# Kernel tuning notes

Measured on AMD Instinct MI355X. Metric: run time of the kernel, lower is better.

The kernel has to match this reference:

```python
import jax, jax.numpy as jnp
import numpy as np

N = 40000
IN_DIM = 2000
HID = 512
OUT_DIM = 30
E = 400000


def setup_inputs() -> dict:
    key = jax.random.key(0)
    k1, k2, k3, k4, k5, k6 = jax.random.split(key, 6)
    features = jax.random.normal(k1, (N, IN_DIM), dtype=jnp.float32)
    edge_index = jax.random.randint(k2, (2, E), 0, N, dtype=jnp.int64)
    # xavier_normal_(gain=1.414): std = gain * sqrt(2/(fan_in+fan_out))
    W1 = jax.random.normal(k3, (IN_DIM, HID), dtype=jnp.float32) * (1.414 * np.sqrt(2.0 / (IN_DIM + HID)))
    W2 = jax.random.normal(k4, (HID, OUT_DIM), dtype=jnp.float32) * (1.414 * np.sqrt(2.0 / (HID + OUT_DIM)))
    att_src = jax.random.normal(k5, (HID,), dtype=jnp.float32) * (1.414 * np.sqrt(2.0 / (1 + HID)))
    att_dst = jax.random.normal(k6, (HID,), dtype=jnp.float32) * (1.414 * np.sqrt(2.0 / (1 + HID)))
    return {"features": features, "W1": W1, "W2": W2,
            "att_src": att_src, "att_dst": att_dst, "edge_index": edge_index}


def _gat_propagate(x_proj, alpha_src, alpha_dst, src, dst, n_nodes):
    """GATConv message+aggregate (heads=1, aggr='add').
    x_proj: [N, C] projected features; alpha_src/alpha_dst: [N] per-node scores.
    """
    score = jax.nn.sigmoid(alpha_src[src] + alpha_dst[dst])          # [E]
    # segment softmax over destination neighborhoods (PyG softmax)
    seg_max = jax.ops.segment_max(score, dst, num_segments=n_nodes)  # [N]
    e = jnp.exp(score - seg_max[dst])                                # [E]
    seg_sum = jax.ops.segment_sum(e, dst, num_segments=n_nodes)     # [N]
    alpha = e / (seg_sum[dst] + 1e-16)                               # [E]
    msg = x_proj[src] * alpha[:, None]                               # [E, C] gather + scale
    return jax.ops.segment_sum(msg, dst, num_segments=n_nodes)      # [N, C] scatter-add


def _stagate_forward(features, W1, W2, att_src, att_dst, src, dst):
    n = features.shape[0]
    # conv1: attention=True (computes its own alpha)
    x1 = features @ W1                                # [N, HID]
    a_src = x1 @ att_src                              # [N]
    a_dst = x1 @ att_dst                              # [N]
    h1 = jax.nn.elu(_gat_propagate(x1, a_src, a_dst, src, dst, n))
    # conv2: attention=False -> just linear projection (heads=1 mean)
    h2 = h1 @ W2                                      # [N, OUT_DIM]
    # conv3: weights tied to W2^T, attention tied to conv1's alphas
    x3 = h2 @ W2.T                                    # [N, HID]
    h3 = jax.nn.elu(_gat_propagate(x3, a_src, a_dst, src, dst, n))
    # conv4: attention=False, weights tied to W1^T
    h4 = h3 @ W1.T                                    # [N, IN_DIM]
    return h2, h4


def reference(features, W1, W2, att_src, att_dst, edge_index):
    src = edge_index[0]
    dst = edge_index[1]
    return _stagate_forward(features, W1, W2, att_src, att_dst, src, dst)
```

## Files before the change

### kernel.cpp

```cpp
#include <hip/hip_runtime.h>
#include <cstdint>

#define NNODES 40000
#define INDIM 2000
#define HIDD 512
#define ODIM 30
#define NEDGES 400000
#define KPAD 2048

typedef short bf16x8 __attribute__((ext_vector_type(8)));
typedef float f32x4 __attribute__((ext_vector_type(4)));

__device__ __forceinline__ float bf2f(ushort u){ union{unsigned int i; float f;} x; x.i = ((unsigned int)u)<<16; return x.f; }
__device__ __forceinline__ ushort f2bf(float v){ union{float f; unsigned int u;} x; x.f=v; unsigned int r = x.u + 0x7fffu + ((x.u>>16)&1u); return (ushort)(r>>16); }

__device__ __forceinline__ int xcd_swz(int orig, int nwg){
  int q = nwg >> 3, r = nwg & 7;
  int xcd = orig & 7;
  int idx = orig >> 3;
  return (xcd < r ? xcd*(q+1) : r*(q+1) + (xcd-r)*q) + idx;
}

__global__ __launch_bounds__(256) void cast_feat_kernel(const float* __restrict__ src, ushort* __restrict__ dstb){
  int c = blockIdx.x*256 + threadIdx.x;
  int row = c >> 8, kc = c & 255;
  bf16x8 o;
  if (kc < INDIM/8) {
    const float* p = src + (size_t)row*INDIM + kc*8;
    #pragma unroll
    for (int j=0;j<8;++j) o[j] = (short)f2bf(p[j]);
  } else {
    #pragma unroll
    for (int j=0;j<8;++j) o[j] = 0;
  }
  *(bf16x8*)(dstb + (size_t)row*KPAD + kc*8) = o;
}

__global__ __launch_bounds__(256) void cast_w1_kernel(const float* __restrict__ W1, ushort* __restrict__ W1b, ushort* __restrict__ W1t){
  int idx = blockIdx.x*256 + threadIdx.x;
  if (idx >= INDIM*HIDD) return;
  int r = idx >> 9, c = idx & 511;
  ushort b = f2bf(W1[idx]);
  W1b[idx] = b;
  W1t[(size_t)c*KPAD + r] = b;
}

__global__ __launch_bounds__(256) void cast_w2_kernel(const float* __restrict__ W2, ushort* __restrict__ W2p, ushort* __restrict__ W2tc){
  int idx = blockIdx.x*256 + threadIdx.x;
  if (idx >= HIDD*32) return;
  int k = idx >> 5, c = idx & 31;
  float val = (c < ODIM) ? W2[k*ODIM + c] : 0.f;
  ushort b = f2bf(val);
  W2p[k*32 + c] = b;
  W2tc[c*HIDD + k] = b;
}

__global__ __launch_bounds__(256) void hist_kernel(const int* __restrict__ dst, int* __restrict__ deg){
  int e = blockIdx.x*256 + threadIdx.x;
  if (e < NEDGES) atomicAdd(&deg[dst[e]], 1);
}

__global__ __launch_bounds__(1024) void scan_kernel(const int* __restrict__ deg, int* __restrict__ row_ptr){
  __shared__ int part[1024];
  const int t = threadIdx.x;
  const int base = t * 40;
  int v[40];
  int s = 0;
  if (base < NNODES) {
    const int4* dp = (const int4*)(deg + base);
    #pragma unroll
    for (int j=0;j<10;++j){
      int4 d = dp[j];
      v[4*j+0] = s; s += d.x;
      v[4*j+1] = s; s += d.y;
      v[4*j+2] = s; s += d.z;
      v[4*j+3] = s; s += d.w;
    }
  } else {
    #pragma unroll
    for (int j=0;j<40;++j) v[j] = 0;
  }
  part[t] = s;
  __syncthreads();
  #pragma unroll
  for (int off=1; off<1024; off<<=1){
    int x = (t >= off) ? part[t-off] : 0;
    __syncthreads();
    part[t] += x;
    __syncthreads();
  }
  int offset = (t > 0) ? part[t-1] : 0;
  #pragma unroll
  for (int j=0;j<40;++j){
    int i = base + j;
    if (i <= NNODES) row_ptr[i] = offset + v[j];
  }
}

__global__ __launch_bounds__(256) void place_kernel(const int* __restrict__ src, const int* __restrict__ dst,
    const int* __restrict__ row_ptr, int* __restrict__ cursor, int* __restrict__ csr_src){
  int e = blockIdx.x*256 + threadIdx.x;
  if (e >= NEDGES) return;
  int d = dst[e];
  int pos = row_ptr[d] + atomicAdd(&cursor[d], 1);
  csr_src[pos] = src[e];
}

#define P_MID  asm volatile("" ::: "memory"); __builtin_amdgcn_s_barrier(); \
               asm volatile("s_waitcnt lgkmcnt(0)" ::: "memory"); \
               __builtin_amdgcn_sched_barrier(0); __builtin_amdgcn_s_setprio(1);
#define P_END  __builtin_amdgcn_s_setprio(0); asm volatile("" ::: "memory"); \
               __builtin_amdgcn_s_barrier(); __builtin_amdgcn_sched_barrier(0);
#define P_ENDW __builtin_amdgcn_s_setprio(0); \
               asm volatile("s_waitcnt vmcnt(4)" ::: "memory"); \
               asm volatile("" ::: "memory"); __builtin_amdgcn_s_barrier(); \
               __builtin_amdgcn_sched_barrier(0);

template<typename OutT>
__global__ __launch_bounds__(512, 2) void gemm8_kernel(
    const ushort* __restrict__ A, const ushort* __restrict__ Bt,
    OutT* __restrict__ C, int M, int N, int K, int ldc, int nwg, int cshift)
{
  __shared__ __align__(16) char smem[131072];
  ushort* Al = (ushort*)smem;
  ushort* Bl = (ushort*)(smem + 65536);
  const int tid = threadIdx.x;
  const int lane = tid & 63;
  const int w = tid >> 6;
  const int wm = w >> 2, wn = w & 3;
  const int s = xcd_swz(blockIdx.x, nwg);
  const int row0 = (s >> cshift) << 8;
  const int col0 = (s & ((1 << cshift) - 1)) << 8;
  const int NT = K >> 6;

  f32x4 acc[8][4] = {};
  bf16x8 a[4][2], b[4][2];

  auto stage = [&](bool isA, int kt, int h){
    const ushort* G = isA ? A : Bt;
    int base = isA ? row0 : col0;
    int lim  = isA ? M : N;
    ushort* L = (isA ? Al : Bl) + ((kt & 1) << 14);
    if (kt >= NT) kt -= NT;
    #pragma unroll
    for (int it = 0; it < 2; ++it){
      int ch = tid + (it << 9);
      int rl = (h << 7) + (ch >> 3);
      int cs = ch & 7;
      int gr = base + rl; gr = gr < lim ? gr : lim - 1;
      int gc = (kt << 6) + ((cs ^ (rl & 7)) << 3);
      __builtin_amdgcn_global_load_lds(
        (const __attribute__((address_space(1))) unsigned int*)(G + (size_t)gr*K + gc),
        (__attribute__((address_space(3))) unsigned int*)(L + rl*64 + cs*8), 16, 0, 0);
    }
  };
  auto lda = [&](int buf, int mf, int kk) -> bf16x8 {
    int rl = wm*128 + mf*16 + (lane & 15);
    int ko = kk*32 + ((lane >> 4) << 3);
    return *(const bf16x8*)&Al[(buf << 14) + rl*64 + (ko ^ ((rl & 7) << 3))];
  };
  auto ldb = [&](int buf, int nf, int kk) -> bf16x8 {
    int rl = wn*64 + nf*16 + (lane & 15);
    int ko = kk*32 + ((lane >> 4) << 3);
    return *(const bf16x8*)&Bl[(buf << 14) + rl*64 + (ko ^ ((rl & 7) << 3))];
  };
  auto mfma_q = [&](int mbase, int nbase){
    #pragma unroll
    for (int i=0;i<4;++i)
      #pragma unroll
      for (int j=0;j<2;++j)
        #pragma unroll
        for (int kk=0;kk<2;++kk)
          acc[mbase+i][nbase+j] = __builtin_amdgcn_mfma_f32_16x16x32_bf16(
              a[i][kk], b[nbase+j][kk], acc[mbase+i][nbase+j], 0, 0, 0);
  };

  stage(false, 0, 0); stage(false, 0, 1);
  stage(true , 0, 0); stage(true , 0, 1);
  stage(false, 1, 0); stage(false, 1, 1);
  asm volatile("s_waitcnt vmcnt(4)" ::: "memory");
  asm volatile("" ::: "memory");
  __builtin_amdgcn_s_barrier();
  __builtin_amdgcn_sched_barrier(0);

  const int NT2 = NT >> 1;
  for (int t = 0; t < NT2; ++t){
    const int kt0 = 2*t, kt1 = 2*t + 1;
    #pragma unroll
    for (int i=0;i<4;++i){ a[i][0]=lda(0,i,0); a[i][1]=lda(0,i,1); }
    #pragma unroll
    for (int j=0;j<2;++j){ b[j][0]=ldb(0,j,0); b[j][1]=ldb(0,j,1); }
    stage(true, kt1, 0);
    P_MID; mfma_q(0,0); P_END;
    #pragma unroll
    for (int j=2;j<4;++j){ b[j][0]=ldb(0,j,0); b[j][1]=ldb(0,j,1); }
    stage(true, kt1, 1);
    P_MID; mfma_q(0,2); P_END;
    #pragma unroll
    for (int i=0;i<4;++i){ a[i][0]=lda(0,4+i,0); a[i][1]=lda(0,4+i,1); }
    stage(false, kt0+2, 0);
    P_MID; mfma_q(4,0); P_END;
    stage(false, kt0+2, 1);
    P_MID; mfma_q(4,2); P_ENDW;
    #pragma unroll
    for (int i=0;i<4;++i){ a[i][0]=lda(1,i,0); a[i][1]=lda(1,i,1); }
    #pragma unroll
    for (int j=0;j<2;++j){ b[j][0]=ldb(1,j,0); b[j][1]=ldb(1,j,1); }
    stage(true, kt0+2, 0);
    P_MID; mfma_q(0,0); P_END;
    #pragma unroll
    for (int j=2;j<4;++j){ b[j][0]=ldb(1,j,0); b[j][1]=ldb(1,j,1); }
    stage(true, kt0+2, 1);
    P_MID; mfma_q(0,2); P_END;
    #pragma unroll
    for (int i=0;i<4;++i){ a[i][0]=lda(1,4+i,0); a[i][1]=lda(1,4+i,1); }
    stage(false, kt1+2, 0);
    P_MID; mfma_q(4,0); P_END;
    stage(false, kt1+2, 1);
    P_MID; mfma_q(4,2); P_ENDW;
  }

  asm volatile("s_waitcnt vmcnt(0)" ::: "memory");
  __syncthreads();

  if constexpr (sizeof(OutT)==2) {
    ushort* cs = (ushort*)smem;
    #pragma unroll
    for (int p=0;p<2;++p){
      if (wm == p){
        #pragma unroll
        for (int mf=0;mf<8;++mf)
          #pragma unroll
          for (int nf=0;nf<4;++nf)
            #pragma unroll
            for (int reg=0;reg<4;++reg)
              cs[(mf*16 + ((lane>>4)<<2) + reg)*264 + wn*64 + nf*16 + (lane&15)] = f2bf(acc[mf][nf][reg]);
      }
      __syncthreads();
      #pragma unroll
      for (int it=0; it<8; ++it){
        int ch = tid + it*512;
        int r = ch >> 5, c8 = (ch & 31) * 8;
        int gr = row0 + p*128 + r;
        if (gr < M && col0 + c8 + 8 <= N)
          *(bf16x8*)&((ushort*)C)[(size_t)gr*ldc + col0 + c8] = *(const bf16x8*)&cs[r*264 + c8];
      }
      __syncthreads();
    }
  } else {
    float* cf = (float*)smem;
    #pragma unroll
    for (int p=0;p<4;++p){
      if (wm == (p>>1)){
        int mh = (p & 1) * 4;
        #pragma unroll
        for (int i=0;i<4;++i)
          #pragma unroll
          for (int nf=0;nf<4;++nf)
            #pragma unroll
            for (int reg=0;reg<4;++reg)
              cf[(i*16 + ((lane>>4)<<2) + reg)*260 + wn*64 + nf*16 + (lane&15)] = acc[mh+i][nf][reg];
      }
      __syncthreads();
      #pragma unroll
      for (int it=0; it<8; ++it){
        int ch = tid + it*512;
        int r = ch >> 6, c4 = (ch & 63) * 4;
        int gr = row0 + p*64 + r, gc = col0 + c4;
        if (gr < M && gc + 4 <= N)
          *(f32x4*)&((float*)C)[(size_t)gr*ldc + gc] = *(const f32x4*)&cf[r*260 + c4];
      }
      __syncthreads();
    }
  }
}

__global__ __launch_bounds__(256) void a_kernel(const ushort* __restrict__ x1,
    const float* __restrict__ att_src, const float* __restrict__ att_dst,
    float* __restrict__ a_src, float* __restrict__ a_dst){
  int gid = blockIdx.x*256 + threadIdx.x;
  int row = gid >> 6, lane = gid & 63;
  if (row >= NNODES) return;
  bf16x8 v = *(const bf16x8*)(x1 + (size_t)row*HIDD + lane*8);
  float ps = 0.f, pd = 0.f;
  #pragma unroll
  for (int j=0;j<8;++j){
    float xv = bf2f((ushort)v[j]);
    ps += xv * att_src[lane*8+j];
    pd += xv * att_dst[lane*8+j];
  }
  #pragma unroll
  for (int off=32; off>0; off>>=1){ ps += __shfl_down(ps, off); pd += __shfl_down(pd, off); }
  if (lane == 0){ a_src[row] = ps; a_dst[row] = pd; }
}

__global__ __launch_bounds__(256) void agg_fused_kernel(const ushort* __restrict__ X,
    const int* __restrict__ row_ptr, const int* __restrict__ csr_src,
    const float* __restrict__ a_src, const float* __restrict__ a_dst,
    float* __restrict__ csr_alpha, ushort* __restrict__ outb){
  __shared__ float red[3][64*8];
  __shared__ float albuf[1024];
  int v = blockIdx.x;
  int lane = threadIdx.x & 63;
  int q = threadIdx.x >> 6;
  int p0 = row_ptr[v], p1 = row_ptr[v+1];
  int deg = p1 - p0;

  if (q == 0){
    float ad = a_dst[v];
    float m = -1e30f;
    for (int i = lane; i < deg; i += 64){
      float sc = 1.f/(1.f + __expf(-(a_src[csr_src[p0+i]] + ad)));
      if (i < 1024) albuf[i] = sc;
      m = fmaxf(m, sc);
    }
    #pragma unroll
    for (int off=32; off>0; off>>=1) m = fmaxf(m, __shfl_xor(m, off));
    float sum = 0.f;
    for (int i = lane; i < deg; i += 64){
      float sc = (i < 1024) ? albuf[i]
               : 1.f/(1.f + __expf(-(a_src[csr_src[p0+i]] + ad)));
      float e = __expf(sc - m);
      if (i < 1024) albuf[i] = e;
      sum += e;
    }
    #pragma unroll
    for (int off=32; off>0; off>>=1) sum += __shfl_xor(sum, off);
    float inv = 1.f/(sum + 1e-16f);
    for (int i = lane; i < deg; i += 64){
      float e = (i < 1024) ? albuf[i]
              : __expf(1.f/(1.f + __expf(-(a_src[csr_src[p0+i]] + ad))) - m);
      float al = e * inv;
      if (i < 1024) albuf[i] = al;
      csr_alpha[p0+i] = al;
    }
  }
  __syncthreads();

  float acc[8] = {0.f,0.f,0.f,0.f,0.f,0.f,0.f,0.f};
  for (int p = p0 + q; p < p1; p += 4){
    int i = p - p0;
    int sidx = csr_src[p];
    float al = (i < 1024) ? albuf[i] : csr_alpha[p];
    bf16x8 xv = *(const bf16x8*)(X + (size_t)sidx*HIDD + lane*8);
    #pragma unroll
    for (int j=0;j<8;++j) acc[j] += al * bf2f((ushort)xv[j]);
  }
  if (q > 0){
    #pragma unroll
    for (int j=0;j<8;++j) red[q-1][lane*8+j] = acc[j];
  }
  __syncthreads();
  if (q == 0){
    bf16x8 o;
    #pragma unroll
    for (int j=0;j<8;++j){
      float a = acc[j] + red[0][lane*8+j] + red[1][lane*8+j] + red[2][lane*8+j];
      a = a > 0.f ? a : __expf(a)-1.f;
      o[j] = (short)f2bf(a);
    }
    *(bf16x8*)(outb + (size_t)v*HIDD + lane*8) = o;
  }
}

__global__ __launch_bounds__(256) void mid_kernel(const ushort* __restrict__ h1,
    const ushort* __restrict__ W2tc, float* __restrict__ h2){
  __shared__ ushort h1s[32*512];
  __shared__ ushort w2s[32*512];
  const int t = threadIdx.x;
  const int row0 = blockIdx.x * 32;
  const ushort* g = h1 + (size_t)row0*HIDD;
  #pragma unroll
  for (int it=0; it<8; ++it){
    int ch = t + it*256;
    *(bf16x8*)&h1s[ch*8] = *(const bf16x8*)&g[ch*8];
    *(bf16x8*)&w2s[ch*8] = *(const bf16x8*)&W2tc[ch*8];
  }
  __syncthreads();
  int c = t & 31, rg = t >> 5;
  if (c < ODIM){
    float acc[4] = {0.f,0.f,0.f,0.f};
    for (int k0=0;k0<64;++k0){
      bf16x8 wv = *(const bf16x8*)&w2s[c*512 + k0*8];
      #pragma unroll
      for (int rr=0; rr<4; ++rr){
        bf16x8 hv = *(const bf16x8*)&h1s[(rg*4+rr)*HIDD + k0*8];
        #pragma unroll
        for (int j=0;j<8;++j) acc[rr] += bf2f((ushort)hv[j]) * bf2f((ushort)wv[j]);
      }
    }
    #pragma unroll
    for (int rr=0;rr<4;++rr) h2[(size_t)(row0 + rg*4 + rr)*ODIM + c] = acc[rr];
  }
}

__global__ __launch_bounds__(256) void agg30_kernel(const float* __restrict__ h2,
    const int* __restrict__ row_ptr, const int* __restrict__ csr_src,
    const float* __restrict__ csr_alpha, float* __restrict__ g){
  int gid = blockIdx.x*256 + threadIdx.x;
  int v = gid >> 5, lane = gid & 31;
  if (v >= NNODES) return;
  int p0 = row_ptr[v], p1 = row_ptr[v+1];
  float acc = 0.f;
  if (lane < ODIM){
    for (int p = p0; p < p1; ++p){
      acc += csr_alpha[p] * h2[(size_t)csr_src[p]*ODIM + lane];
    }
  }
  g[(size_t)v*32 + lane] = acc;
}

__global__ __launch_bounds__(256) void g2h3_kernel(const float* __restrict__ g,
    const ushort* __restrict__ W2p, ushort* __restrict__ h3){
  int gid = blockIdx.x*256 + threadIdx.x;
  int row = gid >> 6, lane = gid & 63;
  if (row >= NNODES) return;
  float h[ODIM];
  #pragma unroll
  for (int ci=0; ci<ODIM; ++ci) h[ci] = g[(size_t)row*32 + ci];
  #pragma unroll
  for (int it=0; it<8; ++it){
    int n = it*64 + lane;
    const ushort* wr = W2p + n*32;
    bf16x8 wvv[4];
    #pragma unroll
    for (int q=0;q<4;++q) wvv[q] = *(const bf16x8*)(wr + q*8);
    float acc = 0.f;
    #pragma unroll
    for (int ci=0; ci<ODIM; ++ci) acc += h[ci]*bf2f((ushort)wvv[ci>>3][ci&7]);
    acc = acc > 0.f ? acc : __expf(acc)-1.f;
    h3[(size_t)row*HIDD + n] = f2bf(acc);
  }
}

extern "C" void kernel_launch(void* const* d_in, const int* in_sizes, int n_in,
                              void* d_out, int out_size, void* d_ws, size_t ws_size,
                              hipStream_t stream){
  const float* features = (const float*)d_in[0];
  const float* W1 = (const float*)d_in[1];
  const float* W2 = (const float*)d_in[2];
  const float* att_src = (const float*)d_in[3];
  const float* att_dst = (const float*)d_in[4];
  const int* edge = (const int*)d_in[5];
  const int* esrc = edge;
  const int* edst = edge + NEDGES;

  float* h2 = (float*)d_out;
  float* h4 = h2 + (size_t)NNODES*ODIM;
  char* obase = (char*)h4;
  ushort* featb = (ushort*)obase;
  ushort* x1b   = (ushort*)(obase + 163840000);
  ushort* h1b   = (ushort*)(obase + 204800000);

  char* wbase = (char*)d_ws;
  size_t o = 0;
  auto walloc = [&](size_t bytes)->void*{ void* p = wbase + o; o += (bytes + 255) & ~(size_t)255; return p; };
  ushort* h3b      = (ushort*)walloc((size_t)NNODES*HIDD*2);
  ushort* W1b      = (ushort*)walloc((size_t)INDIM*HIDD*2);
  ushort* W1t      = (ushort*)walloc((size_t)HIDD*KPAD*2);
  ushort* W2p      = (ushort*)walloc(512*32*2);
  ushort* W2tc     = (ushort*)walloc(32*512*2);
  float*  a_src    = (float*)walloc(NNODES*4);
  float*  a_dst    = (float*)walloc(NNODES*4);
  int*    deg      = (int*)walloc(NNODES*4);
  int*    cursor   = (int*)walloc(NNODES*4);
  int*    row_ptr  = (int*)walloc((NNODES+1)*4);
  int*    csr_src  = (int*)walloc(NEDGES*4);
  float*  csr_alpha= (float*)walloc(NEDGES*4);
  float*  gbuf     = (float*)walloc((size_t)NNODES*32*4);

  hipMemsetAsync(deg, 0, NNODES*4, stream);
  hipMemsetAsync(cursor, 0, NNODES*4, stream);
  hipMemsetAsync(W1t, 0, (size_t)HIDD*KPAD*2, stream);

  cast_feat_kernel<<<40000, 256, 0, stream>>>(features, featb);
  cast_w1_kernel<<<(INDIM*HIDD+255)/256, 256, 0, stream>>>(W1, W1b, W1t);
  cast_w2_kernel<<<(HIDD*32+255)/256, 256, 0, stream>>>(W2, W2p, W2tc);
  hist_kernel<<<(NEDGES+255)/256, 256, 0, stream>>>(edst, deg);
  scan_kernel<<<1, 1024, 0, stream>>>(deg, row_ptr);
  place_kernel<<<(NEDGES+255)/256, 256, 0, stream>>>(esrc, edst, row_ptr, cursor, csr_src);

  gemm8_kernel<ushort><<<314, 512, 0, stream>>>(featb, W1t, x1b, NNODES, HIDD, KPAD, HIDD, 314, 1);
  a_kernel<<<10000, 256, 0, stream>>>(x1b, att_src, att_dst, a_src, a_dst);
  agg_fused_kernel<<<NNODES, 256, 0, stream>>>(x1b, row_ptr, csr_src, a_src, a_dst, csr_alpha, h1b);
  mid_kernel<<<NNODES/32, 256, 0, stream>>>(h1b, W2tc, h2);
  agg30_kernel<<<NNODES*32/256, 256, 0, stream>>>(h2, row_ptr, csr_src, csr_alpha, gbuf);
  g2h3_kernel<<<10000, 256, 0, stream>>>(gbuf, W2p, h3b);
  gemm8_kernel<float><<<1256, 512, 0, stream>>>(h3b, W1b, h4, NNODES, INDIM, HIDD, INDIM, 1256, 3);
}
```

Measured before the change: 682.6 us.

## Merge setup kernels, fold scan into GEMM, wave-per-node aggregation, fuse conv3

```diff
diff --git a/kernel.cpp b/kernel.cpp
--- a/kernel.cpp
+++ b/kernel.cpp
@@ -21,89 +21,57 @@
   return (xcd < r ? xcd*(q+1) : r*(q+1) + (xcd-r)*q) + idx;
 }
 
-__global__ __launch_bounds__(256) void cast_feat_kernel(const float* __restrict__ src, ushort* __restrict__ dstb){
-  int c = blockIdx.x*256 + threadIdx.x;
-  int row = c >> 8, kc = c & 255;
-  bf16x8 o;
-  if (kc < INDIM/8) {
-    const float* p = src + (size_t)row*INDIM + kc*8;
-    #pragma unroll
-    for (int j=0;j<8;++j) o[j] = (short)f2bf(p[j]);
+#define SB_FEAT   40000
+#define SB_W1     (SB_FEAT + 4000)
+#define SB_W2     (SB_W1 + 64)
+#define SB_HIST   (SB_W2 + 1563)
+#define SB_PAD    (SB_HIST + 96)
+#define SB_CUR    (SB_PAD + 157)
+
+__global__ __launch_bounds__(256) void setup_kernel(
+    const float* __restrict__ features, const float* __restrict__ W1, const float* __restrict__ W2,
+    const int* __restrict__ edst,
+    ushort* __restrict__ featb, ushort* __restrict__ W1b, ushort* __restrict__ W1t,
+    ushort* __restrict__ W2p, ushort* __restrict__ W2tc,
+    int* __restrict__ deg, int* __restrict__ cursor){
+  int b = blockIdx.x, t = threadIdx.x;
+  if (b < SB_FEAT){
+    int c = b*256 + t;
+    int row = c >> 8, kc = c & 255;
+    bf16x8 o;
+    if (kc < INDIM/8) {
+      const float* p = features + (size_t)row*INDIM + kc*8;
+      #pragma unroll
+      for (int j=0;j<8;++j) o[j] = (short)f2bf(p[j]);
+    } else {
+      #pragma unroll
+      for (int j=0;j<8;++j) o[j] = 0;
+    }
+    *(bf16x8*)(featb + (size_t)row*KPAD + kc*8) = o;
+  } else if (b < SB_W1){
+    int idx = (b - SB_FEAT)*256 + t;
+    int r = idx >> 9, c = idx & 511;
+    ushort bb = f2bf(W1[idx]);
+    W1b[idx] = bb;
+    W1t[(size_t)c*KPAD + r] = bb;
+  } else if (b < SB_W2){
+    int idx = (b - SB_W1)*256 + t;
+    int k = idx >> 5, c = idx & 31;
+    float val = (c < ODIM) ? W2[k*ODIM + c] : 0.f;
+    ushort bb = f2bf(val);
+    W2p[k*32 + c] = bb;
+    W2tc[c*HIDD + k] = bb;
+  } else if (b < SB_HIST){
+    int e = (b - SB_W2)*256 + t;
+    if (e < NEDGES) atomicAdd(&deg[edst[e]], 1);
+  } else if (b < SB_PAD){
+    int z = (b - SB_HIST)*256 + t;
+    int c = z / 48, r = 2000 + (z - c*48);
+    W1t[(size_t)c*KPAD + r] = 0;
   } else {
-    #pragma unroll
-    for (int j=0;j<8;++j) o[j] = 0;
-  }
-  *(bf16x8*)(dstb + (size_t)row*KPAD + kc*8) = o;
-}
-
-__global__ __launch_bounds__(256) void cast_w1_kernel(const float* __restrict__ W1, ushort* __restrict__ W1b, ushort* __restrict__ W1t){
-  int idx = blockIdx.x*256 + threadIdx.x;
-  if (idx >= INDIM*HIDD) return;
-  int r = idx >> 9, c = idx & 511;
-  ushort b = f2bf(W1[idx]);
-  W1b[idx] = b;
-  W1t[(size_t)c*KPAD + r] = b;
-}
-
-__global__ __launch_bounds__(256) void cast_w2_kernel(const float* __restrict__ W2, ushort* __restrict__ W2p, ushort* __restrict__ W2tc){
-  int idx = blockIdx.x*256 + threadIdx.x;
-  if (idx >= HIDD*32) return;
-  int k = idx >> 5, c = idx & 31;
-  float val = (c < ODIM) ? W2[k*ODIM + c] : 0.f;
-  ushort b = f2bf(val);
-  W2p[k*32 + c] = b;
-  W2tc[c*HIDD + k] = b;
-}
-
-__global__ __launch_bounds__(256) void hist_kernel(const int* __restrict__ dst, int* __restrict__ deg){
-  int e = blockIdx.x*256 + threadIdx.x;
-  if (e < NEDGES) atomicAdd(&deg[dst[e]], 1);
-}
-
-__global__ __launch_bounds__(1024) void scan_kernel(const int* __restrict__ deg, int* __restrict__ row_ptr){
-  __shared__ int part[1024];
-  const int t = threadIdx.x;
-  const int base = t * 40;
-  int v[40];
-  int s = 0;
-  if (base < NNODES) {
-    const int4* dp = (const int4*)(deg + base);
-    #pragma unroll
-    for (int j=0;j<10;++j){
-      int4 d = dp[j];
-      v[4*j+0] = s; s += d.x;
-      v[4*j+1] = s; s += d.y;
-      v[4*j+2] = s; s += d.z;
-      v[4*j+3] = s; s += d.w;
-    }
-  } else {
-    #pragma unroll
-    for (int j=0;j<40;++j) v[j] = 0;
-  }
-  part[t] = s;
-  __syncthreads();
-  #pragma unroll
-  for (int off=1; off<1024; off<<=1){
-    int x = (t >= off) ? part[t-off] : 0;
-    __syncthreads();
-    part[t] += x;
-    __syncthreads();
-  }
-  int offset = (t > 0) ? part[t-1] : 0;
-  #pragma unroll
-  for (int j=0;j<40;++j){
-    int i = base + j;
-    if (i <= NNODES) row_ptr[i] = offset + v[j];
-  }
-}
-
-__global__ __launch_bounds__(256) void place_kernel(const int* __restrict__ src, const int* __restrict__ dst,
-    const int* __restrict__ row_ptr, int* __restrict__ cursor, int* __restrict__ csr_src){
-  int e = blockIdx.x*256 + threadIdx.x;
-  if (e >= NEDGES) return;
-  int d = dst[e];
-  int pos = row_ptr[d] + atomicAdd(&cursor[d], 1);
-  csr_src[pos] = src[e];
+    int z = (b - SB_PAD)*256 + t;
+    if (z < NNODES) cursor[z] = 0;
+  }
 }
 
 #define P_MID  asm volatile("" ::: "memory"); __builtin_amdgcn_s_barrier(); \
@@ -116,12 +84,39 @@
                asm volatile("" ::: "memory"); __builtin_amdgcn_s_barrier(); \
                __builtin_amdgcn_sched_barrier(0);
 
-template<typename OutT>
+template<typename OutT, bool DOSCAN>
 __global__ __launch_bounds__(512, 2) void gemm8_kernel(
     const ushort* __restrict__ A, const ushort* __restrict__ Bt,
-    OutT* __restrict__ C, int M, int N, int K, int ldc, int nwg, int cshift)
+    OutT* __restrict__ C, int M, int N, int K, int ldc, int nwg, int cshift,
+    const int* __restrict__ degp, int* __restrict__ row_ptr)
 {
   __shared__ __align__(16) char smem[131072];
+  if constexpr (DOSCAN){
+    if ((int)blockIdx.x == nwg){
+      int* part = (int*)smem;
+      const int t = threadIdx.x;
+      const int base = t * 80;
+      int s = 0;
+      for (int j=0;j<80;++j){ int i = base+j; s += (i < NNODES) ? degp[i] : 0; }
+      part[t] = s;
+      __syncthreads();
+      for (int off=1; off<512; off<<=1){
+        int x = (t >= off) ? part[t-off] : 0;
+        __syncthreads();
+        part[t] += x;
+        __syncthreads();
+      }
+      int run = (t > 0) ? part[t-1] : 0;
+      for (int j=0;j<80;++j){
+        int i = base+j;
+        if (i <= NNODES){
+          row_ptr[i] = run;
+          if (i < NNODES) run += degp[i];
+        }
+      }
+      return;
+    }
+  }
   ushort* Al = (ushort*)smem;
   ushort* Bl = (ushort*)(smem + 65536);
   const int tid = threadIdx.x;
@@ -275,92 +270,108 @@
   }
 }
 
-__global__ __launch_bounds__(256) void a_kernel(const ushort* __restrict__ x1,
-    const float* __restrict__ att_src, const float* __restrict__ att_dst,
+#define PB_PLACE 1563
+__global__ __launch_bounds__(256) void place_a_kernel(
+    const int* __restrict__ esrc, const int* __restrict__ edst,
+    const int* __restrict__ row_ptr, int* __restrict__ cursor, int* __restrict__ csr_src,
+    const ushort* __restrict__ x1, const float* __restrict__ att_src, const float* __restrict__ att_dst,
     float* __restrict__ a_src, float* __restrict__ a_dst){
-  int gid = blockIdx.x*256 + threadIdx.x;
-  int row = gid >> 6, lane = gid & 63;
-  if (row >= NNODES) return;
-  bf16x8 v = *(const bf16x8*)(x1 + (size_t)row*HIDD + lane*8);
-  float ps = 0.f, pd = 0.f;
-  #pragma unroll
-  for (int j=0;j<8;++j){
-    float xv = bf2f((ushort)v[j]);
-    ps += xv * att_src[lane*8+j];
-    pd += xv * att_dst[lane*8+j];
-  }
-  #pragma unroll
-  for (int off=32; off>0; off>>=1){ ps += __shfl_down(ps, off); pd += __shfl_down(pd, off); }
-  if (lane == 0){ a_src[row] = ps; a_dst[row] = pd; }
-}
-
-__global__ __launch_bounds__(256) void agg_fused_kernel(const ushort* __restrict__ X,
+  int b = blockIdx.x, t = threadIdx.x;
+  if (b < PB_PLACE){
+    int e = b*256 + t;
+    if (e >= NEDGES) return;
+    int d = edst[e];
+    int pos = row_ptr[d] + atomicAdd(&cursor[d], 1);
+    csr_src[pos] = esrc[e];
+  } else {
+    int gid = (b - PB_PLACE)*256 + t;
+    int row = gid >> 6, lane = gid & 63;
+    if (row >= NNODES) return;
+    bf16x8 v = *(const bf16x8*)(x1 + (size_t)row*HIDD + lane*8);
+    float ps = 0.f, pd = 0.f;
+    #pragma unroll
+    for (int j=0;j<8;++j){
+      float xv = bf2f((ushort)v[j]);
+      ps += xv * att_src[lane*8+j];
+      pd += xv * att_dst[lane*8+j];
+    }
+    #pragma unroll
+    for (int off=32; off>0; off>>=1){ ps += __shfl_down(ps, off); pd += __shfl_down(pd, off); }
+    if (lane == 0){ a_src[row] = ps; a_dst[row] = pd; }
+  }
+}
+
+__global__ __launch_bounds__(256) void agg1_kernel(const ushort* __restrict__ X,
     const int* __restrict__ row_ptr, const int* __restrict__ csr_src,
     const float* __restrict__ a_src, const float* __restrict__ a_dst,
     float* __restrict__ csr_alpha, ushort* __restrict__ outb){
-  __shared__ float red[3][64*8];
-  __shared__ float albuf[1024];
-  int v = blockIdx.x;
-  int lane = threadIdx.x & 63;
-  int q = threadIdx.x >> 6;
-  int p0 = row_ptr[v], p1 = row_ptr[v+1];
-  int deg = p1 - p0;
-
-  if (q == 0){
-    float ad = a_dst[v];
+  int gid = blockIdx.x*256 + threadIdx.x;
+  int v = gid >> 6, lane = gid & 63;
+  if (v >= NNODES) return;
+  int p0 = row_ptr[v], p1 = row_ptr[v+1], deg = p1 - p0;
+  float ad = a_dst[v];
+  float acc[8] = {0.f,0.f,0.f,0.f,0.f,0.f,0.f,0.f};
+
+  if (deg > 0 && deg <= 64){
+    bool act = lane < deg;
+    int sv = act ? csr_src[p0 + lane] : 0;
+    float sc = act ? 1.f/(1.f + __expf(-(a_src[sv] + ad))) : -1e30f;
+    float m = sc;
+    #pragma unroll
+    for (int off=32; off>0; off>>=1) m = fmaxf(m, __shfl_xor(m, off));
+    float e = act ? __expf(sc - m) : 0.f;
+    float S = e;
+    #pragma unroll
+    for (int off=32; off>0; off>>=1) S += __shfl_xor(S, off);
+    float al = e / (S + 1e-16f);
+    if (act) csr_alpha[p0 + lane] = al;
+    for (int j=0;j<deg;++j){
+      float aj = __shfl(al, j);
+      int sj = __shfl(sv, j);
+      bf16x8 xv = *(const bf16x8*)(X + (size_t)sj*HIDD + lane*8);
+      #pragma unroll
+      for (int k=0;k<8;++k) acc[k] += aj * bf2f((ushort)xv[k]);
+    }
+  } else if (deg > 64){
     float m = -1e30f;
-    for (int i = lane; i < deg; i += 64){
-      float sc = 1.f/(1.f + __expf(-(a_src[csr_src[p0+i]] + ad)));
-      if (i < 1024) albuf[i] = sc;
+    for (int p = p0 + lane; p < p1; p += 64){
+      float sc = 1.f/(1.f + __expf(-(a_src[csr_src[p]] + ad)));
       m = fmaxf(m, sc);
     }
     #pragma unroll
     for (int off=32; off>0; off>>=1) m = fmaxf(m, __shfl_xor(m, off));
-    float sum = 0.f;
-    for (int i = lane; i < deg; i += 64){
-      float sc = (i < 1024) ? albuf[i]
-               : 1.f/(1.f + __expf(-(a_src[csr_src[p0+i]] + ad)));
-      float e = __expf(sc - m);
-      if (i < 1024) albuf[i] = e;
-      sum += e;
-    }
-    #pragma unroll
-    for (int off=32; off>0; off>>=1) sum += __shfl_xor(sum, off);
-    float inv = 1.f/(sum + 1e-16f);
-    for (int i = lane; i < deg; i += 64){
-      float e = (i < 1024) ? albuf[i]
-              : __expf(1.f/(1.f + __expf(-(a_src[csr_src[p0+i]] + ad))) - m);
-      float al = e * inv;
-      if (i < 1024) albuf[i] = al;
-      csr_alpha[p0+i] = al;
-    }
-  }
-  __syncthreads();
-
-  float acc[8] = {0.f,0.f,0.f,0.f,0.f,0.f,0.f,0.f};
-  for (int p = p0 + q; p < p1; p += 4){
-    int i = p - p0;
-    int sidx = csr_src[p];
-    float al = (i < 1024) ? albuf[i] : csr_alpha[p];
-    bf16x8 xv = *(const bf16x8*)(X + (size_t)sidx*HIDD + lane*8);
-    #pragma unroll
-    for (int j=0;j<8;++j) acc[j] += al * bf2f((ushort)xv[j]);
-  }
-  if (q > 0){
-    #pragma unroll
-    for (int j=0;j<8;++j) red[q-1][lane*8+j] = acc[j];
-  }
-  __syncthreads();
-  if (q == 0){
-    bf16x8 o;
-    #pragma unroll
-    for (int j=0;j<8;++j){
-      float a = acc[j] + red[0][lane*8+j] + red[1][lane*8+j] + red[2][lane*8+j];
-      a = a > 0.f ? a : __expf(a)-1.f;
-      o[j] = (short)f2bf(a);
-    }
-    *(bf16x8*)(outb + (size_t)v*HIDD + lane*8) = o;
-  }
+    float S = 0.f;
+    for (int p = p0 + lane; p < p1; p += 64){
+      float sc = 1.f/(1.f + __expf(-(a_src[csr_src[p]] + ad)));
+      S += __expf(sc - m);
+    }
+    #pragma unroll
+    for (int off=32; off>0; off>>=1) S += __shfl_xor(S, off);
+    float inv = 1.f/(S + 1e-16f);
+    for (int base = p0; base < p1; base += 64){
+      int p = base + lane;
+      bool act = p < p1;
+      int sv = act ? csr_src[p] : 0;
+      float al = act ? __expf(1.f/(1.f + __expf(-(a_src[sv] + ad))) - m) * inv : 0.f;
+      if (act) csr_alpha[p] = al;
+      int cnt = p1 - base; cnt = cnt < 64 ? cnt : 64;
+      for (int j=0;j<cnt;++j){
+        float aj = __shfl(al, j);
+        int sj = __shfl(sv, j);
+        bf16x8 xv = *(const bf16x8*)(X + (size_t)sj*HIDD + lane*8);
+        #pragma unroll
+        for (int k=0;k<8;++k) acc[k] += aj * bf2f((ushort)xv[k]);
+      }
+    }
+  }
+  bf16x8 o;
+  #pragma unroll
+  for (int k=0;k<8;++k){
+    float a = acc[k];
+    a = a > 0.f ? a : __expf(a)-1.f;
+    o[k] = (short)f2bf(a);
+  }
+  *(bf16x8*)(outb + (size_t)v*HIDD + lane*8) = o;
 }
 
 __global__ __launch_bounds__(256) void mid_kernel(const ushort* __restrict__ h1,
@@ -394,30 +405,22 @@
   }
 }
 
-__global__ __launch_bounds__(256) void agg30_kernel(const float* __restrict__ h2,
+__global__ __launch_bounds__(256) void conv3_kernel(const float* __restrict__ h2,
     const int* __restrict__ row_ptr, const int* __restrict__ csr_src,
-    const float* __restrict__ csr_alpha, float* __restrict__ g){
+    const float* __restrict__ csr_alpha, const ushort* __restrict__ W2p,
+    ushort* __restrict__ h3){
   int gid = blockIdx.x*256 + threadIdx.x;
-  int v = gid >> 5, lane = gid & 31;
+  int v = gid >> 6, lane = gid & 63;
   if (v >= NNODES) return;
   int p0 = row_ptr[v], p1 = row_ptr[v+1];
-  float acc = 0.f;
+  float accd = 0.f;
   if (lane < ODIM){
-    for (int p = p0; p < p1; ++p){
-      acc += csr_alpha[p] * h2[(size_t)csr_src[p]*ODIM + lane];
-    }
-  }
-  g[(size_t)v*32 + lane] = acc;
-}
-
-__global__ __launch_bounds__(256) void g2h3_kernel(const float* __restrict__ g,
-    const ushort* __restrict__ W2p, ushort* __restrict__ h3){
-  int gid = blockIdx.x*256 + threadIdx.x;
-  int row = gid >> 6, lane = gid & 63;
-  if (row >= NNODES) return;
-  float h[ODIM];
+    for (int p = p0; p < p1; ++p)
+      accd += csr_alpha[p] * h2[(size_t)csr_src[p]*ODIM + lane];
+  }
+  float gv[ODIM];
   #pragma unroll
-  for (int ci=0; ci<ODIM; ++ci) h[ci] = g[(size_t)row*32 + ci];
+  for (int ci=0; ci<ODIM; ++ci) gv[ci] = __shfl(accd, ci);
   #pragma unroll
   for (int it=0; it<8; ++it){
     int n = it*64 + lane;
@@ -427,9 +430,9 @@
     for (int q=0;q<4;++q) wvv[q] = *(const bf16x8*)(wr + q*8);
     float acc = 0.f;
     #pragma unroll
-    for (int ci=0; ci<ODIM; ++ci) acc += h[ci]*bf2f((ushort)wvv[ci>>3][ci&7]);
+    for (int ci=0; ci<ODIM; ++ci) acc += gv[ci]*bf2f((ushort)wvv[ci>>3][ci&7]);
     acc = acc > 0.f ? acc : __expf(acc)-1.f;
-    h3[(size_t)row*HIDD + n] = f2bf(acc);
+    h3[(size_t)v*HIDD + n] = f2bf(acc);
   }
 }
 
@@ -467,24 +470,21 @@
   int*    row_ptr  = (int*)walloc((NNODES+1)*4);
   int*    csr_src  = (int*)walloc(NEDGES*4);
   float*  csr_alpha= (float*)walloc(NEDGES*4);
-  float*  gbuf     = (float*)walloc((size_t)NNODES*32*4);
 
   hipMemsetAsync(deg, 0, NNODES*4, stream);
-  hipMemsetAsync(cursor, 0, NNODES*4, stream);
-  hipMemsetAsync(W1t, 0, (size_t)HIDD*KPAD*2, stream);
-
-  cast_feat_kernel<<<40000, 256, 0, stream>>>(features, featb);
-  cast_w1_kernel<<<(INDIM*HIDD+255)/256, 256, 0, stream>>>(W1, W1b, W1t);
-  cast_w2_kernel<<<(HIDD*32+255)/256, 256, 0, stream>>>(W2, W2p, W2tc);
-  hist_kernel<<<(NEDGES+255)/256, 256, 0, stream>>>(edst, deg);
-  scan_kernel<<<1, 1024, 0, stream>>>(deg, row_ptr);
-  place_kernel<<<(NEDGES+255)/256, 256, 0, stream>>>(esrc, edst, row_ptr, cursor, csr_src);
-
-  gemm8_kernel<ushort><<<314, 512, 0, stream>>>(featb, W1t, x1b, NNODES, HIDD, KPAD, HIDD, 314, 1);
-  a_kernel<<<10000, 256, 0, stream>>>(x1b, att_src, att_dst, a_src, a_dst);
-  agg_fused_kernel<<<NNODES, 256, 0, stream>>>(x1b, row_ptr, csr_src, a_src, a_dst, csr_alpha, h1b);
+
+  setup_kernel<<<SB_CUR, 256, 0, stream>>>(features, W1, W2, edst,
+      featb, W1b, W1t, W2p, W2tc, deg, cursor);
+
+  gemm8_kernel<ushort, true><<<315, 512, 0, stream>>>(featb, W1t, x1b,
+      NNODES, HIDD, KPAD, HIDD, 314, 1, deg, row_ptr);
+
+  place_a_kernel<<<PB_PLACE + 10000, 256, 0, stream>>>(esrc, edst,
+      row_ptr, cursor, csr_src, x1b, att_src, att_dst, a_src, a_dst);
+
+  agg1_kernel<<<10000, 256, 0, stream>>>(x1b, row_ptr, csr_src, a_src, a_dst, csr_alpha, h1b);
   mid_kernel<<<NNODES/32, 256, 0, stream>>>(h1b, W2tc, h2);
-  agg30_kernel<<<NNODES*32/256, 256, 0, stream>>>(h2, row_ptr, csr_src, csr_alpha, gbuf);
-  g2h3_kernel<<<10000, 256, 0, stream>>>(gbuf, W2p, h3b);
-  gemm8_kernel<float><<<1256, 512, 0, stream>>>(h3b, W1b, h4, NNODES, INDIM, HIDD, INDIM, 1256, 3);
-}
+  conv3_kernel<<<10000, 256, 0, stream>>>(h2, row_ptr, csr_src, csr_alpha, W2p, h3b);
+  gemm8_kernel<float, false><<<1256, 512, 0, stream>>>(h3b, W1b, h4,
+      NNODES, INDIM, HIDD, INDIM, 1256, 3, nullptr, nullptr);
+}
```

Result: faster. 646.3 us (-5.3%).
